# Kernel tuning notes

Hardware: AMD Instinct MI355X
Metric: run time of the kernel (lower is better)

## Reference

```python
import jax, jax.numpy as jnp
import numpy as np

N, C, H, K = 50000, 256, 8, 16
M = N * K
HID = 4 * C
HD = C // H
SCALE = HD ** -0.5
EPS = 1e-5


def setup_inputs() -> dict:
    key = jax.random.key(0)
    ks = jax.random.split(key, 8)
    init = lambda k, shape, fan: jax.random.normal(k, shape, jnp.float32) * (fan ** -0.5)
    return {
        "feats": jax.random.normal(ks[0], (N, C), jnp.float32),
        "polar_pos": jax.random.normal(ks[1], (N, 3), jnp.float32),
        "edge_index": jax.random.randint(ks[2], (2, M), 0, N, dtype=jnp.int64),
        "ln1_g": jnp.ones((C,), jnp.float32), "ln1_b": jnp.zeros((C,), jnp.float32),
        "qkv_w": init(ks[3], (3 * C, C), C), "qkv_b": jnp.zeros((3 * C,), jnp.float32),
        "proj_w": init(ks[4], (C, C), C), "proj_b": jnp.zeros((C,), jnp.float32),
        "ln2_g": jnp.ones((C,), jnp.float32), "ln2_b": jnp.zeros((C,), jnp.float32),
        "fc1_w": init(ks[5], (HID, C), C), "fc1_b": jnp.zeros((HID,), jnp.float32),
        "fc2_w": init(ks[6], (C, HID), HID), "fc2_b": jnp.zeros((C,), jnp.float32),
    }


def _ln(x, g, b):
    m = x.mean(-1, keepdims=True)
    v = jnp.var(x, axis=-1, keepdims=True)
    return (x - m) * jax.lax.rsqrt(v + EPS) * g + b


def reference(feats, polar_pos, edge_index, ln1_g, ln1_b, qkv_w, qkv_b,
              proj_w, proj_b, ln2_g, ln2_b, fc1_w, fc1_b, fc2_w, fc2_b):
    skip = feats
    x = _ln(feats, ln1_g, ln1_b)

    # edge bookkeeping: sort edges by destination (index_0), matching torch.sort
    idx0 = edge_index[0]
    idx1 = edge_index[1]
    order = jnp.argsort(idx0)  # stable sort
    idx0 = idx0[order]
    idx1 = idx1[order]

    # qkv projection -> (N, 3, H, HD)
    qkv = (x @ qkv_w.T + qkv_b).reshape(N, 3, H, HD)
    q = qkv[:, 0] * SCALE  # (N, H, HD)
    k = qkv[:, 1]
    v = qkv[:, 2]

    # attention_step1_v2: per-edge dot products, (M, H)
    attn = jnp.einsum('mhd,mhd->mh', q[idx0], k[idx1])

    # scatter_softmax over edges grouped by idx0
    mx = jax.ops.segment_max(attn, idx0, num_segments=N)
    e = jnp.exp(attn - mx[idx0])
    s = jax.ops.segment_sum(e, idx0, num_segments=N)
    w = e / s[idx0]  # (M, H)

    # attention_step2: weighted aggregation of neighbor values
    out = jax.ops.segment_sum(w[:, :, None] * v[idx1], idx0, num_segments=N)
    out = out.reshape(N, C)

    out = out @ proj_w.T + proj_b
    feats = skip + out

    y = _ln(feats, ln2_g, ln2_b)
    y = jax.nn.gelu(y @ fc1_w.T + fc1_b, approximate=False)
    y = y @ fc2_w.T + fc2_b
    return feats + y
```

## Files before the change

### kernel.cpp

```cpp
#include <hip/hip_runtime.h>
#include <hip/hip_bf16.h>
#include <cmath>


#define N_NODES 50000
#define C_DIM 256
#define M_EDGES 800000
#define ATT_SCALE 0.17677669529663687f
#define LN_EPS 1e-5f
#define LOG2E 1.4426950408889634f
#define NEG_BIG -3.0e38f

typedef unsigned int uint_t;
typedef unsigned short ushort_t;
typedef short short8 __attribute__((ext_vector_type(8)));
typedef float floatx4 __attribute__((ext_vector_type(4)));

__device__ __forceinline__ ushort_t f2bf(float f) {
  uint_t u = __float_as_uint(f);
  return (ushort_t)((u + 0x7FFFu + ((u >> 16) & 1u)) >> 16);
}
__device__ __forceinline__ float bf_even(uint_t u) { return __uint_as_float(u << 16); }
__device__ __forceinline__ float bf_odd(uint_t u) { return __uint_as_float(u & 0xFFFF0000u); }

__device__ __forceinline__ float gelu_tanh(float x) {
  const float u = 0.7978845608028654f * (x + 0.044715f * x * x * x);
  const float e = __expf(2.0f * u);
  const float t = 1.0f - 2.0f / (e + 1.0f);
  return 0.5f * x * (1.0f + t);
}

__device__ __forceinline__ void gload16(const void* g, void* l) {
  __builtin_amdgcn_global_load_lds(
      (const __attribute__((address_space(1))) void*)g,
      (__attribute__((address_space(3))) void*)l, 16, 0, 0);
}

__global__ __launch_bounds__(256) void ln_kernel(const float* __restrict__ x,
    const float* __restrict__ g, const float* __restrict__ b,
    ushort_t* __restrict__ y)
{
  const int row = blockIdx.x * 4 + (threadIdx.x >> 6);
  const int lane = threadIdx.x & 63;
  const float4 v = *(const float4*)(x + (size_t)row * C_DIM + lane * 4);
  float s = v.x + v.y + v.z + v.w;
  float s2 = v.x * v.x + v.y * v.y + v.z * v.z + v.w * v.w;
#pragma unroll
  for (int m = 1; m < 64; m <<= 1) {
    s += __shfl_xor(s, m);
    s2 += __shfl_xor(s2, m);
  }
  const float mean = s * (1.0f / 256.0f);
  const float var = fmaxf(s2 * (1.0f / 256.0f) - mean * mean, 0.0f);
  const float r = rsqrtf(var + LN_EPS);
  const float4 g4 = *(const float4*)(g + lane * 4);
  const float4 b4 = *(const float4*)(b + lane * 4);
  ushort4 o;
  o.x = f2bf((v.x - mean) * r * g4.x + b4.x);
  o.y = f2bf((v.y - mean) * r * g4.y + b4.y);
  o.z = f2bf((v.z - mean) * r * g4.z + b4.z);
  o.w = f2bf((v.w - mean) * r * g4.w + b4.w);
  *(ushort4*)(y + (size_t)row * C_DIM + lane * 4) = o;
}

__global__ void cvt_kernel(const float* __restrict__ s0, const float* __restrict__ s1,
                           const float* __restrict__ s2, const float* __restrict__ s3,
                           ushort_t* __restrict__ dst)
{
  const int i = blockIdx.x * 256 + threadIdx.x;
  float v;
  if (i < 196608) v = s0[i];
  else if (i < 262144) v = s1[i - 196608];
  else if (i < 524288) v = s2[i - 262144];
  else v = s3[i - 524288];
  dst[i] = f2bf(v);
}

template <int EPI>
__global__ __launch_bounds__(256, 2) void mfma_gemm(
    const ushort_t* __restrict__ A, const ushort_t* __restrict__ W,
    const float* __restrict__ bias, const float* __restrict__ extra,
    void* __restrict__ OutV, int Kdim, int Jdim)
{
  __shared__ __align__(16) char smem[40960];
  ushort_t* As = (ushort_t*)smem;
  ushort_t* Bs = As + 64 * 64;
  const int t = threadIdx.x;
  const int lane = t & 63;
  const int w = t >> 6;
  const int wm = w & 1;
  const int wn = w >> 1;
  const int rowbase = blockIdx.y * 64;
  const int colbase = blockIdx.x * 256;

  floatx4 acc[2][8] = {};

  const int base = w * 64 + lane;
  const int rbase = base >> 3;
  const int kcs = (base & 7) ^ (rbase & 7);

  const int rl = lane & 15;
  const int qd = lane >> 4;

  for (int k0 = 0; k0 < Kdim; k0 += 64) {
#pragma unroll
    for (int h = 0; h < 2; ++h) {
      int grow = rowbase + h * 32 + rbase;
      if (grow > N_NODES - 1) grow = N_NODES - 1;
      gload16(A + (size_t)grow * Kdim + k0 + kcs * 8,
              As + (h * 256 + w * 64) * 8);
    }
#pragma unroll
    for (int h = 0; h < 8; ++h) {
      const int gcol = colbase + h * 32 + rbase;
      gload16(W + (size_t)gcol * Kdim + k0 + kcs * 8,
              Bs + (h * 256 + w * 64) * 8);
    }
    __syncthreads();

#pragma unroll
    for (int h = 0; h < 2; ++h) {
      short8 af[2], bf[8];
#pragma unroll
      for (int tm = 0; tm < 2; ++tm) {
        const int ra = wm * 32 + tm * 16 + rl;
        const int kc = (h * 4 + qd) ^ (ra & 7);
        af[tm] = *(const short8*)(As + ra * 64 + kc * 8);
      }
#pragma unroll
      for (int tn = 0; tn < 8; ++tn) {
        const int rb = wn * 128 + tn * 16 + rl;
        const int kc = (h * 4 + qd) ^ (rb & 7);
        bf[tn] = *(const short8*)(Bs + rb * 64 + kc * 8);
      }
#pragma unroll
      for (int tm = 0; tm < 2; ++tm)
#pragma unroll
        for (int tn = 0; tn < 8; ++tn)
          acc[tm][tn] = __builtin_amdgcn_mfma_f32_16x16x32_bf16(
              af[tm], bf[tn], acc[tm][tn], 0, 0, 0);
    }
    __syncthreads();
  }

  const int rr = lane >> 4;
  if (EPI == 1) {
    float* sc = (float*)smem + w * (32 * 68);
    const int c4 = (lane & 15) * 4;
#pragma unroll
    for (int p = 0; p < 2; ++p) {
      __syncthreads();
#pragma unroll
      for (int th = 0; th < 4; ++th) {
        const int tn = p * 4 + th;
#pragma unroll
        for (int tm = 0; tm < 2; ++tm)
#pragma unroll
          for (int r = 0; r < 4; ++r)
            sc[(tm * 16 + qd * 4 + r) * 68 + th * 16 + rl] = acc[tm][tn][r];
      }
      __syncthreads();
      const int col0 = colbase + wn * 128 + p * 64 + c4;
      const float4 b4 = *(const float4*)(bias + col0);
#pragma unroll
      for (int it = 0; it < 8; ++it) {
        const int lr = it * 4 + rr;
        const int grow = rowbase + wm * 32 + lr;
        if (grow >= N_NODES) continue;
        float4 v = *(const float4*)(sc + lr * 68 + c4);
        const float4 e4 = *(const float4*)(extra + (size_t)grow * Jdim + col0);
        v.x += b4.x + e4.x; v.y += b4.y + e4.y;
        v.z += b4.z + e4.z; v.w += b4.w + e4.w;
        *(float4*)((float*)OutV + (size_t)grow * Jdim + col0) = v;
      }
    }
  } else {
    __syncthreads();
    ushort_t* su = (ushort_t*)smem + w * (32 * 136);
#pragma unroll
    for (int tn = 0; tn < 8; ++tn) {
      const int col = colbase + wn * 128 + tn * 16 + rl;
      const float bv = bias[col];
#pragma unroll
      for (int tm = 0; tm < 2; ++tm)
#pragma unroll
        for (int r = 0; r < 4; ++r) {
          float v = acc[tm][tn][r] + bv;
          if (EPI == 0) {
            if (col < 256) v *= ATT_SCALE;
          } else {
            v = gelu_tanh(v);
          }
          su[(tm * 16 + qd * 4 + r) * 136 + tn * 16 + rl] = f2bf(v);
        }
    }
    __syncthreads();
    const int c8 = (lane & 15) * 8;
#pragma unroll
    for (int it = 0; it < 8; ++it) {
      const int lr = it * 4 + rr;
      const int grow = rowbase + wm * 32 + lr;
      if (grow >= N_NODES) continue;
      const uint4 v = *(const uint4*)(su + lr * 136 + c8);
      *(uint4*)((ushort_t*)OutV + (size_t)grow * Jdim + colbase + wn * 128 + c8) = v;
    }
  }
}

__global__ void hist_kernel(const int* __restrict__ idx0, int* __restrict__ counts)
{
  const int m = blockIdx.x * 256 + threadIdx.x;
  if (m < M_EDGES) atomicAdd(&counts[idx0[m]], 1);
}

__global__ __launch_bounds__(256) void scan1_kernel(const int* __restrict__ counts,
    int* __restrict__ offsets, int* __restrict__ bsums)
{
  __shared__ int tmp[256];
  const int t = threadIdx.x;
  const int i = blockIdx.x * 256 + t;
  const int v = (i < N_NODES) ? counts[i] : 0;
  int x = v;
  tmp[t] = x;
  __syncthreads();
#pragma unroll
  for (int off = 1; off < 256; off <<= 1) {
    const int a = (t >= off) ? tmp[t - off] : 0;
    __syncthreads();
    x += a;
    tmp[t] = x;
    __syncthreads();
  }
  if (i < N_NODES) offsets[i] = x - v;
  if (t == 255) bsums[blockIdx.x] = x;
}

__global__ __launch_bounds__(256) void scan2_kernel(int* __restrict__ bsums, int nb)
{
  __shared__ int tmp[256];
  const int t = threadIdx.x;
  const int v = (t < nb) ? bsums[t] : 0;
  int x = v;
  tmp[t] = x;
  __syncthreads();
#pragma unroll
  for (int off = 1; off < 256; off <<= 1) {
    const int a = (t >= off) ? tmp[t - off] : 0;
    __syncthreads();
    x += a;
    tmp[t] = x;
    __syncthreads();
  }
  if (t < nb) bsums[t] = x - v;
}

__global__ void scan3_kernel(int* __restrict__ offsets, const int* __restrict__ bsums)
{
  const int i = blockIdx.x * 256 + threadIdx.x;
  if (i < N_NODES) offsets[i] += bsums[blockIdx.x];
  if (i == 0) offsets[N_NODES] = M_EDGES;
}

__global__ void scatter_kernel(const int* __restrict__ idx0,
    const int* __restrict__ idx1, const int* __restrict__ offsets,
    int* __restrict__ cursor, int* __restrict__ srcs)
{
  const int m = blockIdx.x * 256 + threadIdx.x;
  if (m < M_EDGES) {
    const int n = idx0[m];
    const int p = offsets[n] + atomicAdd(&cursor[n], 1);
    srcs[p] = idx1[m];
  }
}

__global__ __launch_bounds__(256) void attn_kernel(
    const ushort_t* __restrict__ QKVh, const int* __restrict__ offsets,
    const int* __restrict__ srcs, ushort_t* __restrict__ AO)
{
  const int node = blockIdx.x * 4 + (threadIdx.x >> 6);
  if (node >= N_NODES) return;
  const int lane = threadIdx.x & 63;
  const int h = lane & 7;
  const int slot = lane >> 3;
  const int start = offsets[node];
  const int end = offsets[node + 1];

  float q[32];
  {
    const uint4* qr = (const uint4*)(QKVh + (size_t)node * 768 + h * 32);
#pragma unroll
    for (int i = 0; i < 4; ++i) {
      const uint4 u = qr[i];
      q[i * 8 + 0] = bf_even(u.x); q[i * 8 + 1] = bf_odd(u.x);
      q[i * 8 + 2] = bf_even(u.y); q[i * 8 + 3] = bf_odd(u.y);
      q[i * 8 + 4] = bf_even(u.z); q[i * 8 + 5] = bf_odd(u.z);
      q[i * 8 + 6] = bf_even(u.w); q[i * 8 + 7] = bf_odd(u.w);
    }
  }

  float m = NEG_BIG, s = 0.f;
  float o[32];
#pragma unroll
  for (int d = 0; d < 32; ++d) o[d] = 0.f;

  for (int e = start + slot; e < end; e += 16) {
    const bool has1 = (e + 8) < end;
    const int s0i = srcs[e];
    const int s1i = has1 ? srcs[e + 8] : s0i;
    const uint4* k0p = (const uint4*)(QKVh + (size_t)s0i * 768 + 256 + h * 32);
    const uint4* k1p = (const uint4*)(QKVh + (size_t)s1i * 768 + 256 + h * 32);
    const uint4* v0p = (const uint4*)(QKVh + (size_t)s0i * 768 + 512 + h * 32);
    const uint4* v1p = (const uint4*)(QKVh + (size_t)s1i * 768 + 512 + h * 32);
    uint4 ka[4], kb[4], va[4], vb[4];
#pragma unroll
    for (int i = 0; i < 4; ++i) {
      ka[i] = k0p[i]; kb[i] = k1p[i];
      va[i] = v0p[i]; vb[i] = v1p[i];
    }
    float d0 = 0.f, d1 = 0.f;
#pragma unroll
    for (int i = 0; i < 4; ++i) {
      const uint4 u = ka[i];
      d0 += q[i * 8 + 0] * bf_even(u.x) + q[i * 8 + 1] * bf_odd(u.x);
      d0 += q[i * 8 + 2] * bf_even(u.y) + q[i * 8 + 3] * bf_odd(u.y);
      d0 += q[i * 8 + 4] * bf_even(u.z) + q[i * 8 + 5] * bf_odd(u.z);
      d0 += q[i * 8 + 6] * bf_even(u.w) + q[i * 8 + 7] * bf_odd(u.w);
      const uint4 x = kb[i];
      d1 += q[i * 8 + 0] * bf_even(x.x) + q[i * 8 + 1] * bf_odd(x.x);
      d1 += q[i * 8 + 2] * bf_even(x.y) + q[i * 8 + 3] * bf_odd(x.y);
      d1 += q[i * 8 + 4] * bf_even(x.z) + q[i * 8 + 5] * bf_odd(x.z);
      d1 += q[i * 8 + 6] * bf_even(x.w) + q[i * 8 + 7] * bf_odd(x.w);
    }
    const float l0 = d0 * LOG2E;
    const float l1 = has1 ? d1 * LOG2E : NEG_BIG;
    const float mn = fmaxf(fmaxf(m, l0), l1);
    const float fac = exp2f(m - mn);
    const float w0 = exp2f(l0 - mn);
    const float w1 = has1 ? exp2f(l1 - mn) : 0.f;
    m = mn;
    s = s * fac + w0 + w1;
#pragma unroll
    for (int i = 0; i < 4; ++i) {
      const uint4 ua = va[i];
      const uint4 ub = vb[i];
      o[i * 8 + 0] = o[i * 8 + 0] * fac + w0 * bf_even(ua.x) + w1 * bf_even(ub.x);
      o[i * 8 + 1] = o[i * 8 + 1] * fac + w0 * bf_odd(ua.x)  + w1 * bf_odd(ub.x);
      o[i * 8 + 2] = o[i * 8 + 2] * fac + w0 * bf_even(ua.y) + w1 * bf_even(ub.y);
      o[i * 8 + 3] = o[i * 8 + 3] * fac + w0 * bf_odd(ua.y)  + w1 * bf_odd(ub.y);
      o[i * 8 + 4] = o[i * 8 + 4] * fac + w0 * bf_even(ua.z) + w1 * bf_even(ub.z);
      o[i * 8 + 5] = o[i * 8 + 5] * fac + w0 * bf_odd(ua.z)  + w1 * bf_odd(ub.z);
      o[i * 8 + 6] = o[i * 8 + 6] * fac + w0 * bf_even(ua.w) + w1 * bf_even(ub.w);
      o[i * 8 + 7] = o[i * 8 + 7] * fac + w0 * bf_odd(ua.w)  + w1 * bf_odd(ub.w);
    }
  }

  float mx = m;
  mx = fmaxf(mx, __shfl_xor(mx, 8));
  mx = fmaxf(mx, __shfl_xor(mx, 16));
  mx = fmaxf(mx, __shfl_xor(mx, 32));
  const float fac = exp2f(m - mx);
  s *= fac;
#pragma unroll
  for (int d = 0; d < 32; ++d) o[d] *= fac;

  s += __shfl_xor(s, 8);
  s += __shfl_xor(s, 16);
  s += __shfl_xor(s, 32);

  {
    const bool up = (slot & 4) != 0;
#pragma unroll
    for (int i = 0; i < 16; ++i) {
      const float send = up ? o[i] : o[i + 16];
      const float recv = __shfl_xor(send, 32);
      o[i] = (up ? o[i + 16] : o[i]) + recv;
    }
  }
  {
    const bool up = (slot & 2) != 0;
#pragma unroll
    for (int i = 0; i < 8; ++i) {
      const float send = up ? o[i] : o[i + 8];
      const float recv = __shfl_xor(send, 16);
      o[i] = (up ? o[i + 8] : o[i]) + recv;
    }
  }
  {
    const bool up = (slot & 1) != 0;
#pragma unroll
    for (int i = 0; i < 4; ++i) {
      const float send = up ? o[i] : o[i + 4];
      const float recv = __shfl_xor(send, 8);
      o[i] = (up ? o[i + 4] : o[i]) + recv;
    }
  }
  const int dbase = ((slot & 4) ? 16 : 0) + ((slot & 2) ? 8 : 0) +
                    ((slot & 1) ? 4 : 0);
  const float inv = (end > start) ? 1.0f / s : 0.0f;
  ushort4 st;
  st.x = f2bf(o[0] * inv); st.y = f2bf(o[1] * inv);
  st.z = f2bf(o[2] * inv); st.w = f2bf(o[3] * inv);
  *(ushort4*)(AO + (size_t)node * 256 + h * 32 + dbase) = st;
}

extern "C" void kernel_launch(void* const* d_in, const int* in_sizes, int n_in,
                              void* d_out, int out_size, void* d_ws,
                              size_t ws_size, hipStream_t stream)
{
  const float* feats  = (const float*)d_in[0];
  const int*   edge   = (const int*)d_in[2];
  const float* ln1_g  = (const float*)d_in[3];
  const float* ln1_b  = (const float*)d_in[4];
  const float* qkv_w  = (const float*)d_in[5];
  const float* qkv_b  = (const float*)d_in[6];
  const float* proj_w = (const float*)d_in[7];
  const float* proj_b = (const float*)d_in[8];
  const float* ln2_g  = (const float*)d_in[9];
  const float* ln2_b  = (const float*)d_in[10];
  const float* fc1_w  = (const float*)d_in[11];
  const float* fc1_b  = (const float*)d_in[12];
  const float* fc2_w  = (const float*)d_in[13];
  const float* fc2_b  = (const float*)d_in[14];
  float* out = (float*)d_out;

  ushort_t* Xb   = (ushort_t*)d_ws;
  ushort_t* QKVh = Xb + (size_t)N_NODES * 256;
  ushort_t* AOb  = QKVh + (size_t)N_NODES * 768;
  ushort_t* Hb   = QKVh;
  ushort_t* wb   = AOb + (size_t)N_NODES * 256;
  ushort_t* qkv_wb  = wb;
  ushort_t* proj_wb = qkv_wb + 768 * 256;
  ushort_t* fc1_wb  = proj_wb + 256 * 256;
  ushort_t* fc2_wb  = fc1_wb + 1024 * 256;
  int* counts  = (int*)(fc2_wb + 256 * 1024);
  int* cursor  = counts + N_NODES;
  int* offsets = cursor + N_NODES;
  int* srcs    = offsets + N_NODES + 1;
  int* bsums   = srcs + M_EDGES;
  const size_t required = (size_t)((char*)(bsums + 256) - (char*)d_ws);
  if (ws_size < required) {
    hipMemsetAsync(d_out, 0, (size_t)out_size * sizeof(float), stream);
    return;
  }
  const int* idx0 = edge;
  const int* idx1 = edge + M_EDGES;
  const int rowTiles = (N_NODES + 63) / 64;
  const int scanBlocks = (N_NODES + 255) / 256;

  hipMemsetAsync(counts, 0, 2 * N_NODES * sizeof(int), stream);
  cvt_kernel<<<786432 / 256, 256, 0, stream>>>(qkv_w, proj_w, fc1_w, fc2_w, wb);

  ln_kernel<<<N_NODES / 4, 256, 0, stream>>>(feats, ln1_g, ln1_b, Xb);
  mfma_gemm<0><<<dim3(768 / 256, rowTiles), 256, 0, stream>>>(
      Xb, qkv_wb, qkv_b, nullptr, QKVh, 256, 768);
  hist_kernel<<<(M_EDGES + 255) / 256, 256, 0, stream>>>(idx0, counts);
  scan1_kernel<<<scanBlocks, 256, 0, stream>>>(counts, offsets, bsums);
  scan2_kernel<<<1, 256, 0, stream>>>(bsums, scanBlocks);
  scan3_kernel<<<scanBlocks, 256, 0, stream>>>(offsets, bsums);
  scatter_kernel<<<(M_EDGES + 255) / 256, 256, 0, stream>>>(idx0, idx1, offsets,
                                                            cursor, srcs);
  attn_kernel<<<N_NODES / 4, 256, 0, stream>>>(QKVh, offsets, srcs, AOb);
  mfma_gemm<1><<<dim3(256 / 256, rowTiles), 256, 0, stream>>>(
      AOb, proj_wb, proj_b, feats, out, 256, 256);
  ln_kernel<<<N_NODES / 4, 256, 0, stream>>>(out, ln2_g, ln2_b, Xb);
  mfma_gemm<2><<<dim3(1024 / 256, rowTiles), 256, 0, stream>>>(
      Xb, fc1_wb, fc1_b, nullptr, Hb, 256, 1024);
  mfma_gemm<1><<<dim3(256 / 256, rowTiles), 256, 0, stream>>>(
      Hb, fc2_wb, fc2_b, out, out, 1024, 256);
}
```

Before: 560.1 us.

## Remap attention lanes to split channels across lanes with coalesced K/V row loads

The attention kernel now assigns each lane 8 contiguous channels, so 32 lanes cover a full 256-channel row and the two wave halves process alternating edges. Each K/V row load is therefore one coalesced 512-byte access rather than eight lanes each reading 64 bytes of a different head. Per-head dot products are reduced with two xor shuffles, and the final merge across halves is a single shuffle step instead of the multi-stage cross-slot reduction. Register use drops from 32+32 floats to 8. Separately, the GEMM launch bounds are raised to 3 blocks per CU, which may force register spills.

New measurement: 554.6 us. Within noise of the previous version (-1.0%).

```diff
diff --git a/kernel.cpp b/kernel.cpp
--- a/kernel.cpp
+++ b/kernel.cpp
@@ -77,7 +77,7 @@
 }
 
 template <int EPI>
-__global__ __launch_bounds__(256, 2) void mfma_gemm(
+__global__ __launch_bounds__(256, 3) void mfma_gemm(
     const ushort_t* __restrict__ A, const ushort_t* __restrict__ W,
     const float* __restrict__ bias, const float* __restrict__ extra,
     void* __restrict__ OutV, int Kdim, int Jdim)
@@ -280,127 +280,80 @@
   const int node = blockIdx.x * 4 + (threadIdx.x >> 6);
   if (node >= N_NODES) return;
   const int lane = threadIdx.x & 63;
-  const int h = lane & 7;
-  const int slot = lane >> 3;
+  const int l32 = lane & 31;
+  const int half = lane >> 5;
   const int start = offsets[node];
   const int end = offsets[node + 1];
 
-  float q[32];
-  {
-    const uint4* qr = (const uint4*)(QKVh + (size_t)node * 768 + h * 32);
-#pragma unroll
-    for (int i = 0; i < 4; ++i) {
-      const uint4 u = qr[i];
-      q[i * 8 + 0] = bf_even(u.x); q[i * 8 + 1] = bf_odd(u.x);
-      q[i * 8 + 2] = bf_even(u.y); q[i * 8 + 3] = bf_odd(u.y);
-      q[i * 8 + 4] = bf_even(u.z); q[i * 8 + 5] = bf_odd(u.z);
-      q[i * 8 + 6] = bf_even(u.w); q[i * 8 + 7] = bf_odd(u.w);
-    }
-  }
+  const uint4 qp = *(const uint4*)((const uint_t*)(QKVh + (size_t)node * 768) + l32 * 4);
 
   float m = NEG_BIG, s = 0.f;
-  float o[32];
-#pragma unroll
-  for (int d = 0; d < 32; ++d) o[d] = 0.f;
-
-  for (int e = start + slot; e < end; e += 16) {
-    const bool has1 = (e + 8) < end;
-    const int s0i = srcs[e];
-    const int s1i = has1 ? srcs[e + 8] : s0i;
-    const uint4* k0p = (const uint4*)(QKVh + (size_t)s0i * 768 + 256 + h * 32);
-    const uint4* k1p = (const uint4*)(QKVh + (size_t)s1i * 768 + 256 + h * 32);
-    const uint4* v0p = (const uint4*)(QKVh + (size_t)s0i * 768 + 512 + h * 32);
-    const uint4* v1p = (const uint4*)(QKVh + (size_t)s1i * 768 + 512 + h * 32);
-    uint4 ka[4], kb[4], va[4], vb[4];
-#pragma unroll
-    for (int i = 0; i < 4; ++i) {
-      ka[i] = k0p[i]; kb[i] = k1p[i];
-      va[i] = v0p[i]; vb[i] = v1p[i];
-    }
-    float d0 = 0.f, d1 = 0.f;
-#pragma unroll
-    for (int i = 0; i < 4; ++i) {
-      const uint4 u = ka[i];
-      d0 += q[i * 8 + 0] * bf_even(u.x) + q[i * 8 + 1] * bf_odd(u.x);
-      d0 += q[i * 8 + 2] * bf_even(u.y) + q[i * 8 + 3] * bf_odd(u.y);
-      d0 += q[i * 8 + 4] * bf_even(u.z) + q[i * 8 + 5] * bf_odd(u.z);
-      d0 += q[i * 8 + 6] * bf_even(u.w) + q[i * 8 + 7] * bf_odd(u.w);
-      const uint4 x = kb[i];
-      d1 += q[i * 8 + 0] * bf_even(x.x) + q[i * 8 + 1] * bf_odd(x.x);
-      d1 += q[i * 8 + 2] * bf_even(x.y) + q[i * 8 + 3] * bf_odd(x.y);
-      d1 += q[i * 8 + 4] * bf_even(x.z) + q[i * 8 + 5] * bf_odd(x.z);
-      d1 += q[i * 8 + 6] * bf_even(x.w) + q[i * 8 + 7] * bf_odd(x.w);
-    }
-    const float l0 = d0 * LOG2E;
-    const float l1 = has1 ? d1 * LOG2E : NEG_BIG;
-    const float mn = fmaxf(fmaxf(m, l0), l1);
+  float o[8];
+#pragma unroll
+  for (int j = 0; j < 8; ++j) o[j] = 0.f;
+
+  for (int e = start + half; e < end; e += 4) {
+    const int eB = e + 2;
+    const bool hasB = eB < end;
+    const int sA = srcs[e];
+    const int sB = srcs[hasB ? eB : e];
+    const uint_t* rA = (const uint_t*)(QKVh + (size_t)sA * 768);
+    const uint_t* rB = (const uint_t*)(QKVh + (size_t)sB * 768);
+    const uint4 kA = *(const uint4*)(rA + 128 + l32 * 4);
+    const uint4 kB = *(const uint4*)(rB + 128 + l32 * 4);
+    const uint4 vA = *(const uint4*)(rA + 256 + l32 * 4);
+    const uint4 vB = *(const uint4*)(rB + 256 + l32 * 4);
+
+    float dA = bf_even(qp.x) * bf_even(kA.x) + bf_odd(qp.x) * bf_odd(kA.x)
+             + bf_even(qp.y) * bf_even(kA.y) + bf_odd(qp.y) * bf_odd(kA.y)
+             + bf_even(qp.z) * bf_even(kA.z) + bf_odd(qp.z) * bf_odd(kA.z)
+             + bf_even(qp.w) * bf_even(kA.w) + bf_odd(qp.w) * bf_odd(kA.w);
+    dA += __shfl_xor(dA, 1);
+    dA += __shfl_xor(dA, 2);
+    float dB = bf_even(qp.x) * bf_even(kB.x) + bf_odd(qp.x) * bf_odd(kB.x)
+             + bf_even(qp.y) * bf_even(kB.y) + bf_odd(qp.y) * bf_odd(kB.y)
+             + bf_even(qp.z) * bf_even(kB.z) + bf_odd(qp.z) * bf_odd(kB.z)
+             + bf_even(qp.w) * bf_even(kB.w) + bf_odd(qp.w) * bf_odd(kB.w);
+    dB += __shfl_xor(dB, 1);
+    dB += __shfl_xor(dB, 2);
+
+    const float lA = dA * LOG2E;
+    const float lB = hasB ? dB * LOG2E : NEG_BIG;
+    const float mn = fmaxf(m, fmaxf(lA, lB));
     const float fac = exp2f(m - mn);
-    const float w0 = exp2f(l0 - mn);
-    const float w1 = has1 ? exp2f(l1 - mn) : 0.f;
+    const float wA = exp2f(lA - mn);
+    const float wB = hasB ? exp2f(lB - mn) : 0.f;
     m = mn;
-    s = s * fac + w0 + w1;
-#pragma unroll
-    for (int i = 0; i < 4; ++i) {
-      const uint4 ua = va[i];
-      const uint4 ub = vb[i];
-      o[i * 8 + 0] = o[i * 8 + 0] * fac + w0 * bf_even(ua.x) + w1 * bf_even(ub.x);
-      o[i * 8 + 1] = o[i * 8 + 1] * fac + w0 * bf_odd(ua.x)  + w1 * bf_odd(ub.x);
-      o[i * 8 + 2] = o[i * 8 + 2] * fac + w0 * bf_even(ua.y) + w1 * bf_even(ub.y);
-      o[i * 8 + 3] = o[i * 8 + 3] * fac + w0 * bf_odd(ua.y)  + w1 * bf_odd(ub.y);
-      o[i * 8 + 4] = o[i * 8 + 4] * fac + w0 * bf_even(ua.z) + w1 * bf_even(ub.z);
-      o[i * 8 + 5] = o[i * 8 + 5] * fac + w0 * bf_odd(ua.z)  + w1 * bf_odd(ub.z);
-      o[i * 8 + 6] = o[i * 8 + 6] * fac + w0 * bf_even(ua.w) + w1 * bf_even(ub.w);
-      o[i * 8 + 7] = o[i * 8 + 7] * fac + w0 * bf_odd(ua.w)  + w1 * bf_odd(ub.w);
-    }
-  }
-
-  float mx = m;
-  mx = fmaxf(mx, __shfl_xor(mx, 8));
-  mx = fmaxf(mx, __shfl_xor(mx, 16));
-  mx = fmaxf(mx, __shfl_xor(mx, 32));
-  const float fac = exp2f(m - mx);
-  s *= fac;
-#pragma unroll
-  for (int d = 0; d < 32; ++d) o[d] *= fac;
-
-  s += __shfl_xor(s, 8);
-  s += __shfl_xor(s, 16);
-  s += __shfl_xor(s, 32);
-
-  {
-    const bool up = (slot & 4) != 0;
-#pragma unroll
-    for (int i = 0; i < 16; ++i) {
-      const float send = up ? o[i] : o[i + 16];
-      const float recv = __shfl_xor(send, 32);
-      o[i] = (up ? o[i + 16] : o[i]) + recv;
-    }
-  }
-  {
-    const bool up = (slot & 2) != 0;
-#pragma unroll
-    for (int i = 0; i < 8; ++i) {
-      const float send = up ? o[i] : o[i + 8];
-      const float recv = __shfl_xor(send, 16);
-      o[i] = (up ? o[i + 8] : o[i]) + recv;
-    }
-  }
-  {
-    const bool up = (slot & 1) != 0;
-#pragma unroll
-    for (int i = 0; i < 4; ++i) {
-      const float send = up ? o[i] : o[i + 4];
-      const float recv = __shfl_xor(send, 8);
-      o[i] = (up ? o[i + 4] : o[i]) + recv;
-    }
-  }
-  const int dbase = ((slot & 4) ? 16 : 0) + ((slot & 2) ? 8 : 0) +
-                    ((slot & 1) ? 4 : 0);
-  const float inv = (end > start) ? 1.0f / s : 0.0f;
-  ushort4 st;
-  st.x = f2bf(o[0] * inv); st.y = f2bf(o[1] * inv);
-  st.z = f2bf(o[2] * inv); st.w = f2bf(o[3] * inv);
-  *(ushort4*)(AO + (size_t)node * 256 + h * 32 + dbase) = st;
+    s = s * fac + wA + wB;
+    o[0] = o[0] * fac + wA * bf_even(vA.x) + wB * bf_even(vB.x);
+    o[1] = o[1] * fac + wA * bf_odd(vA.x)  + wB * bf_odd(vB.x);
+    o[2] = o[2] * fac + wA * bf_even(vA.y) + wB * bf_even(vB.y);
+    o[3] = o[3] * fac + wA * bf_odd(vA.y)  + wB * bf_odd(vB.y);
+    o[4] = o[4] * fac + wA * bf_even(vA.z) + wB * bf_even(vB.z);
+    o[5] = o[5] * fac + wA * bf_odd(vA.z)  + wB * bf_odd(vB.z);
+    o[6] = o[6] * fac + wA * bf_even(vA.w) + wB * bf_even(vB.w);
+    o[7] = o[7] * fac + wA * bf_odd(vA.w)  + wB * bf_odd(vB.w);
+  }
+
+  const float mO = __shfl_xor(m, 32);
+  const float sO = __shfl_xor(s, 32);
+  const float mm = fmaxf(m, mO);
+  const float fS = exp2f(m - mm);
+  const float fO = exp2f(mO - mm);
+  const float st = s * fS + sO * fO;
+  float out[8];
+#pragma unroll
+  for (int j = 0; j < 8; ++j) out[j] = o[j] * fS + __shfl_xor(o[j], 32) * fO;
+
+  const float inv = (end > start) ? 1.0f / st : 0.0f;
+  if (lane < 32) {
+    uint4 st4;
+    st4.x = (uint_t)f2bf(out[0] * inv) | ((uint_t)f2bf(out[1] * inv) << 16);
+    st4.y = (uint_t)f2bf(out[2] * inv) | ((uint_t)f2bf(out[3] * inv) << 16);
+    st4.z = (uint_t)f2bf(out[4] * inv) | ((uint_t)f2bf(out[5] * inv) << 16);
+    st4.w = (uint_t)f2bf(out[6] * inv) | ((uint_t)f2bf(out[7] * inv) << 16);
+    *(uint4*)((uint_t*)(AO + (size_t)node * 256) + l32 * 4) = st4;
+  }
 }
 
 extern "C" void kernel_launch(void* const* d_in, const int* in_sizes, int n_in,
```
